# Kernel tuning notes

Measured on AMD Instinct MI355X. Metric: run time of the kernel, lower is better.

The kernel has to match this reference:

```python
import jax, jax.numpy as jnp
import numpy as np

B, S, D = 4, 2048, 1024
H = 16
HD = D // H

def setup_inputs() -> dict:
    key = jax.random.key(0)
    ks = jax.random.split(key, 6)
    std = 1.0 / np.sqrt(D)
    x = jax.random.normal(ks[0], (B, S, D), dtype=jnp.float32)
    Wq = jax.random.uniform(ks[1], (D, D), jnp.float32, -std, std)
    Wk = jax.random.uniform(ks[2], (D, D), jnp.float32, -std, std)
    Wv = jax.random.uniform(ks[3], (D, D), jnp.float32, -std, std)
    Wo = jax.random.uniform(ks[4], (D, D), jnp.float32, -std, std)
    bo = jax.random.uniform(ks[5], (D,), jnp.float32, -std, std)
    return {"x": x, "Wq": Wq, "Wk": Wk, "Wv": Wv, "Wo": Wo, "bo": bo}

def reference(x, Wq, Wk, Wv, Wo, bo):
    b, s, _ = x.shape
    # projections; torch Linear computes x @ W^T, here W stored as (d_in, d_out)... we use (D, D) applied as x @ W
    q = (x @ Wq).reshape(b, s, H, HD).transpose(0, 2, 1, 3)  # b h s hd
    k = (x @ Wk).reshape(b, s, H, HD).transpose(0, 2, 1, 3)
    v = (x @ Wv).reshape(b, s, H, HD).transpose(0, 2, 1, 3)
    scores = jnp.einsum('bhqd,bhkd->bhqk', q, k)
    causal = jnp.triu(jnp.ones((s, s), dtype=bool), k=1)
    scores = jnp.where(causal[None, None], -jnp.inf, scores)
    attn = jax.nn.softmax(scores / np.sqrt(HD), axis=-1)  # dropout=0.0 -> identity
    ctx = jnp.einsum('bhqk,bhkd->bhqd', attn, v)
    ctx = ctx.transpose(0, 2, 1, 3).reshape(b, s, D)
    return ctx @ Wo + bo
```

## Files before the change

kernel.cpp:

```cpp
#include <hip/hip_runtime.h>

typedef unsigned short u16;
typedef __bf16 bf16x8 __attribute__((ext_vector_type(8)));
typedef float f32x4 __attribute__((ext_vector_type(4)));

#define Bn 4
#define Sn 2048
#define Dn 1024
#define Hn 16
#define HDn 64

__device__ inline u16 f2bf(float f) {
  unsigned u = __builtin_bit_cast(unsigned, f);
  u += 0x7fffu + ((u >> 16) & 1u);
  return (u16)(u >> 16);
}

__device__ __forceinline__ void gl2lds16(const u16* g, u16* l) {
  __builtin_amdgcn_global_load_lds(
      (const __attribute__((address_space(1))) unsigned int*)g,
      (__attribute__((address_space(3))) unsigned int*)l, 16, 0, 0);
}

__device__ __forceinline__ float fexp2(float x) {
  return __builtin_amdgcn_exp2f(x);
}

__device__ __forceinline__ unsigned pk_bf_trunc(float lo, float hi) {
  return __builtin_amdgcn_perm(__builtin_bit_cast(unsigned, hi),
                               __builtin_bit_cast(unsigned, lo), 0x07060302u);
}

__global__ __launch_bounds__(256) void cvt4(const float* __restrict__ in,
                                            u16* __restrict__ out, int n4) {
  int i = blockIdx.x * 256 + threadIdx.x;
  if (i < n4) {
    float4 v = ((const float4*)in)[i];
    ushort4 o;
    o.x = f2bf(v.x); o.y = f2bf(v.y); o.z = f2bf(v.z); o.w = f2bf(v.w);
    ((ushort4*)out)[i] = o;
  }
}

__global__ __launch_bounds__(256) void tcvt4(const float* __restrict__ w0,
                                             const float* __restrict__ w1,
                                             const float* __restrict__ w2,
                                             const float* __restrict__ w3,
                                             u16* __restrict__ out) {
  __shared__ u16 tile[32][33];
  const float* in = (blockIdx.z == 0) ? w0 : (blockIdx.z == 1) ? w1
                   : (blockIdx.z == 2) ? w2 : w3;
  u16* dst = out + (size_t)blockIdx.z * Dn * Dn;
  int bx = blockIdx.x * 32;
  int by = blockIdx.y * 32;
  int tx = threadIdx.x & 31;
  int ty = threadIdx.x >> 5;
#pragma unroll
  for (int r = 0; r < 32; r += 8)
    tile[ty + r][tx] = f2bf(in[(size_t)(by + ty + r) * Dn + bx + tx]);
  __syncthreads();
#pragma unroll
  for (int r = 0; r < 32; r += 8)
    dst[(size_t)(bx + ty + r) * Dn + by + tx] = tile[tx][ty + r];
}

#define MFMA16(a, b, c) __builtin_amdgcn_mfma_f32_16x16x32_bf16(a, b, c, 0, 0, 0)

#define SRCP_INIT(APTR, BPTR)                                                \
  const u16* srcp[3][2];                                                     \
  _Pragma("unroll") for (int rg = 0; rg < 3; rg++) {                         \
    _Pragma("unroll") for (int j = 0; j < 2; j++) {                          \
      int o = j * 8192 + tid * 16;                                           \
      int l = o ^ (((o >> 8) & 7) << 4);                                     \
      int rho = l >> 7;                                                      \
      int c2 = (l >> 1) & 63;                                                \
      int gr;                                                                \
      if (rg == 0)      gr = bm + rho;                                       \
      else if (rg == 1) gr = bn + ((rho >> 5) << 6) + (rho & 31);            \
      else              gr = bn + ((rho >> 5) << 6) + 32 + (rho & 31);       \
      const u16* base = (rg == 0) ? (APTR) : (BPTR);                         \
      srcp[rg][j] = base + (size_t)gr * Dn + c2;                             \
    }                                                                        \
  }

#define ARD(D, Q, F, K)                                                      \
  (*(const bf16x8*)((const char*)&S[D][0][0] +                               \
      ((wr * 64 + (Q) * 32 + (F) * 16 + lcol) * 128 + ((K) ? cs1 : cs0))))
#define BRD(D, NI, K)                                                        \
  (*(const bf16x8*)((const char*)&S[D][1 + ((NI) >> 1)][0] +                 \
      ((wc * 32 + ((NI) & 1) * 16 + lcol) * 128 + ((K) ? cs1 : cs0))))

#define VM6 asm volatile("s_waitcnt vmcnt(6)" ::: "memory")
#define VM0 asm volatile("s_waitcnt vmcnt(0)" ::: "memory")

#define KTILE(D, DN, T, WAIT)                                                \
  {                                                                          \
    stg(0, DN, (T) + 2); stg(1, DN, (T) + 2); stg(2, DN, (T) + 2);           \
    __builtin_amdgcn_sched_barrier(0);                                       \
    bf16x8 a00 = ARD(D, 0, 0, 0), a10 = ARD(D, 0, 1, 0);                     \
    bf16x8 a20 = ARD(D, 1, 0, 0), a30 = ARD(D, 1, 1, 0);                     \
    bf16x8 bk0[4], bk1[4];                                                   \
    _Pragma("unroll") for (int ni = 0; ni < 4; ni++) bk0[ni] = BRD(D, ni, 0);\
    bf16x8 a01 = ARD(D, 0, 0, 1), a11 = ARD(D, 0, 1, 1);                     \
    bf16x8 a21 = ARD(D, 1, 0, 1), a31 = ARD(D, 1, 1, 1);                     \
    _Pragma("unroll") for (int ni = 0; ni < 4; ni++) bk1[ni] = BRD(D, ni, 1);\
    __builtin_amdgcn_s_setprio(1);                                           \
    _Pragma("unroll") for (int ni = 0; ni < 4; ni++) {                       \
      acc[0][ni] = MFMA16(a00, bk0[ni], acc[0][ni]);                         \
      acc[1][ni] = MFMA16(a10, bk0[ni], acc[1][ni]);                         \
      acc[2][ni] = MFMA16(a20, bk0[ni], acc[2][ni]);                         \
      acc[3][ni] = MFMA16(a30, bk0[ni], acc[3][ni]);                         \
    }                                                                        \
    _Pragma("unroll") for (int ni = 0; ni < 4; ni++) {                       \
      acc[0][ni] = MFMA16(a01, bk1[ni], acc[0][ni]);                         \
      acc[1][ni] = MFMA16(a11, bk1[ni], acc[1][ni]);                         \
      acc[2][ni] = MFMA16(a21, bk1[ni], acc[2][ni]);                         \
      acc[3][ni] = MFMA16(a31, bk1[ni], acc[3][ni]);                         \
    }                                                                        \
    __builtin_amdgcn_s_setprio(0);                                           \
    WAIT;                                                                    \
    __builtin_amdgcn_s_barrier();                                            \
    __builtin_amdgcn_sched_barrier(0);                                       \
  }

#define KLOOP                                                                \
  stg(0, 0, 0); stg(1, 0, 0); stg(2, 0, 0);                                  \
  stg(0, 1, 1); stg(1, 1, 1); stg(2, 1, 1);                                  \
  VM6;                                                                       \
  __builtin_amdgcn_s_barrier();                                              \
  __builtin_amdgcn_sched_barrier(0);                                         \
  _Pragma("unroll 1") for (int I = 0; I < 5; ++I) {                          \
    const int T0 = 3 * I;                                                    \
    KTILE(0, 2, T0, VM6)                                                     \
    KTILE(1, 0, T0 + 1, VM6)                                                 \
    KTILE(2, 1, T0 + 2, if (I == 4) { VM0; } else { VM6; })                  \
  }                                                                          \
  KTILE(0, 2, 15, )

__global__ __launch_bounds__(512, 2) void gemm_qkv(const u16* __restrict__ A,
                                                   const u16* __restrict__ Bt,
                                                   u16* __restrict__ qkb,
                                                   u16* __restrict__ vt,
                                                   float qscale) {
  __shared__ __attribute__((aligned(16))) u16 S[3][3][8192];

  const int tid = threadIdx.x;
  const int lane = tid & 63;
  const int lcol = lane & 15;
  const int quad = lane >> 4;
  const int wave = tid >> 6;
  const int wr = wave >> 2;
  const int wc = wave & 3;

  const int bid = blockIdx.x;
  const int idx = bid >> 3;
  const int bm = (((bid & 7) << 3) + (idx & 7)) * 128;
  const int bn = (idx >> 3) * 256;

  SRCP_INIT(A, Bt)

  auto stg = [&](int rg, int buf, int tile) {
    if (tile >= 16) return;
    const int k0 = tile << 6;
    u16* d = &S[buf][rg][tid * 8];
    gl2lds16(srcp[rg][0] + k0, d);
    gl2lds16(srcp[rg][1] + k0, d + 4096);
  };

  f32x4 acc[4][4];
#pragma unroll
  for (int i = 0; i < 4; i++)
#pragma unroll
    for (int j = 0; j < 4; j++) acc[i][j] = (f32x4){0.f, 0.f, 0.f, 0.f};

  const int SW = (lcol & 14) << 3;
  const int cs0 = (quad * 16) ^ SW;
  const int cs1 = (64 + quad * 16) ^ SW;

  KLOOP

  const int rb = bm + wr * 64 + quad * 4;
  const int cb = bn + wc * 64 + lcol;
  if (bn >= 2048) {
#pragma unroll
    for (int mi = 0; mi < 4; mi++) {
#pragma unroll
      for (int ni = 0; ni < 4; ni++) {
        int row0 = rb + mi * 16;
        int s = row0 & (Sn - 1);
        int bb = row0 >> 11;
        int vcol = cb + ni * 16 - 2048;
        int bh = (bb << 4) + (vcol >> 6);
        int hd = vcol & 63;
        unsigned d0 = (unsigned)f2bf(acc[mi][ni][0]) |
                      ((unsigned)f2bf(acc[mi][ni][1]) << 16);
        unsigned d1 = (unsigned)f2bf(acc[mi][ni][2]) |
                      ((unsigned)f2bf(acc[mi][ni][3]) << 16);
        *(uint2*)(vt + ((size_t)bh * HDn + hd) * Sn + s) = (uint2){d0, d1};
      }
    }
  } else {
    const float scale = (bn < 1024) ? qscale : 1.0f;
#pragma unroll
    for (int mi = 0; mi < 4; mi++) {
#pragma unroll
      for (int ni = 0; ni < 4; ni++) {
        int row0 = rb + mi * 16;
        int col = cb + ni * 16;
#pragma unroll
        for (int r = 0; r < 4; r++)
          qkb[(size_t)(row0 + r) * 2048 + col] = f2bf(acc[mi][ni][r] * scale);
      }
    }
  }
}

__global__ __launch_bounds__(512, 2) void gemm_out(const u16* __restrict__ A,
                                                   const u16* __restrict__ Bt,
                                                   float* __restrict__ Cout,
                                                   const float* __restrict__ bias) {
  __shared__ __attribute__((aligned(16))) u16 S[3][3][8192];

  const int tid = threadIdx.x;
  const int lane = tid & 63;
  const int lcol = lane & 15;
  const int quad = lane >> 4;
  const int wave = tid >> 6;
  const int wr = wave >> 2;
  const int wc = wave & 3;

  const int bid = blockIdx.x;
  const int idx = bid >> 3;
  const int bm = (((bid & 7) << 3) + (idx & 7)) * 128;
  const int bn = (idx >> 3) * 256;

  SRCP_INIT(A, Bt)

  auto stg = [&](int rg, int buf, int tile) {
    if (tile >= 16) return;
    const int k0 = tile << 6;
    u16* d = &S[buf][rg][tid * 8];
    gl2lds16(srcp[rg][0] + k0, d);
    gl2lds16(srcp[rg][1] + k0, d + 4096);
  };

  f32x4 acc[4][4];
#pragma unroll
  for (int i = 0; i < 4; i++)
#pragma unroll
    for (int j = 0; j < 4; j++) acc[i][j] = (f32x4){0.f, 0.f, 0.f, 0.f};

  const int SW = (lcol & 14) << 3;
  const int cs0 = (quad * 16) ^ SW;
  const int cs1 = (64 + quad * 16) ^ SW;

  KLOOP

  const int rb = bm + wr * 64 + quad * 4;
  const int cb = bn + wc * 64 + lcol;
  float bv[4];
#pragma unroll
  for (int ni = 0; ni < 4; ni++) bv[ni] = bias[cb + ni * 16];
#pragma unroll
  for (int mi = 0; mi < 4; mi++) {
#pragma unroll
    for (int ni = 0; ni < 4; ni++) {
      int row0 = rb + mi * 16;
      int col = cb + ni * 16;
#pragma unroll
      for (int r = 0; r < 4; r++)
        Cout[(size_t)(row0 + r) * Dn + col] = acc[mi][ni][r] + bv[ni];
    }
  }
}

__global__ __launch_bounds__(256, 2) void attn5(const u16* __restrict__ QK,
                                                const u16* __restrict__ Vt,
                                                u16* __restrict__ ctx) {
  __shared__ __attribute__((aligned(16))) u16 Ks2[2][2][64][32];
  __shared__ __attribute__((aligned(16))) u16 Vts2[2][2][64][32];
  __shared__ __attribute__((aligned(16))) u16 Pt[2][4][32][72];

  const int bh = blockIdx.x;
  const int b = bh >> 4, h = bh & 15;
  const int pair = blockIdx.y;
  const int t = threadIdx.x;
  const int w = t >> 6;
  const int lane = t & 63;
  const int lcol = lane & 15;
  const int quad = lane >> 4;
  const int qw0 = pair * 128 + w * 32;
  const int qw1 = (15 - pair) * 128 + w * 32;

  const size_t qkbase = ((size_t)b * Sn) * 2048 + h * HDn;
  const size_t obase = ((size_t)b * Sn) * Dn + h * HDn;
  const size_t vbase = ((size_t)bh * HDn) * Sn;

  bf16x8 qf[2][2][2];
#pragma unroll
  for (int si = 0; si < 2; si++) {
    const int qws = si ? qw1 : qw0;
#pragma unroll
    for (int qb = 0; qb < 2; qb++) {
      const u16* qp = QK + qkbase + (size_t)(qws + qb * 16 + lcol) * 2048 + quad * 8;
      qf[si][qb][0] = *(const bf16x8*)qp;
      qf[si][qb][1] = *(const bf16x8*)(qp + 32);
    }
  }

  bf16x8 onesf;
#pragma unroll
  for (int i = 0; i < 8; i++) onesf[i] = (__bf16)1.0f;

  f32x4 o[2][2][4];
  f32x4 ls[2][2];
#pragma unroll
  for (int si = 0; si < 2; si++) {
#pragma unroll
    for (int qb = 0; qb < 2; qb++) {
      ls[si][qb] = (f32x4){0.f, 0.f, 0.f, 0.f};
#pragma unroll
      for (int nb = 0; nb < 4; nb++) o[si][qb][nb] = (f32x4){0.f, 0.f, 0.f, 0.f};
    }
  }

  const int srow = lane >> 2;
  const int sseg = ((lane & 3) ^ ((lane >> 3) & 3)) * 8;
  const u16* kp0 = QK + qkbase + 1024 + (size_t)(w * 16 + srow) * 2048 + sseg;
  const u16* vp0 = Vt + vbase + (size_t)(w * 16 + srow) * Sn + sseg;
  u16* ksl = &Ks2[0][0][0][0] + w * 512 + lane * 8;
  u16* vsl = &Vts2[0][0][0][0] + w * 512 + lane * 8;

  const int rsw = (quad ^ ((lcol >> 1) & 3)) * 8;

  auto stg_kv = [&](int bs, int j0) {
    const u16* kp = kp0 + (size_t)j0 * 2048;
    const u16* vp = vp0 + j0;
    u16* kd = ksl + bs * 4096;
    u16* vd = vsl + bs * 4096;
    gl2lds16(kp, kd);
    gl2lds16(kp + 32, kd + 2048);
    gl2lds16(vp, vd);
    gl2lds16(vp + 32, vd + 2048);
  };

  auto qk_strip = [&](int si, f32x4 (*s)[2], int bs) {
    __builtin_amdgcn_s_setprio(1);
#pragma unroll
    for (int mb = 0; mb < 4; mb++) {
      bf16x8 kf0 = *(const bf16x8*)(&Ks2[bs][0][mb * 16 + lcol][rsw]);
      bf16x8 kf1 = *(const bf16x8*)(&Ks2[bs][1][mb * 16 + lcol][rsw]);
#pragma unroll
      for (int qb = 0; qb < 2; qb++) {
        f32x4 a = (f32x4){0.f, 0.f, 0.f, 0.f};
        a = MFMA16(kf0, qf[si][qb][0], a);
        a = MFMA16(kf1, qf[si][qb][1], a);
        s[mb][qb] = a;
      }
    }
    __builtin_amdgcn_s_setprio(0);
  };

  auto sm_strip = [&](int si, int qw, int j0, f32x4 (*s)[2]) {
    const bool needmask = (j0 + 63 > qw);
#pragma unroll
    for (int qb = 0; qb < 2; qb++) {
      const int qrow = qw + qb * 16 + lcol;
#pragma unroll
      for (int mb = 0; mb < 4; mb++) {
        float p[4];
#pragma unroll
        for (int r = 0; r < 4; r++) p[r] = fexp2(s[mb][qb][r]);
        if (needmask) {
          const int kvb = j0 + mb * 16 + quad * 4;
#pragma unroll
          for (int r = 0; r < 4; r++)
            if (kvb + r > qrow) p[r] = 0.f;
        }
        unsigned d0 = pk_bf_trunc(p[0], p[1]);
        unsigned d1 = pk_bf_trunc(p[2], p[3]);
        *(uint2*)(&Pt[si][w][qb * 16 + lcol][mb * 16 + quad * 4]) = (uint2){d0, d1};
      }
    }
  };

  auto pv_strip = [&](int si, int bs) {
    __builtin_amdgcn_s_setprio(1);
#pragma unroll
    for (int c = 0; c < 2; c++) {
      bf16x8 pf0 = *(const bf16x8*)(&Pt[si][w][lcol][c * 32 + quad * 8]);
      bf16x8 pf1 = *(const bf16x8*)(&Pt[si][w][16 + lcol][c * 32 + quad * 8]);
      ls[si][0] = MFMA16(onesf, pf0, ls[si][0]);
      ls[si][1] = MFMA16(onesf, pf1, ls[si][1]);
#pragma unroll
      for (int nb = 0; nb < 4; nb++) {
        bf16x8 vf = *(const bf16x8*)(&Vts2[bs][c][nb * 16 + lcol][rsw]);
        o[si][0][nb] = MFMA16(vf, pf0, o[si][0][nb]);
        o[si][1][nb] = MFMA16(vf, pf1, o[si][1][nb]);
      }
    }
    __builtin_amdgcn_s_setprio(0);
  };

  const int n_kv = (15 - pair) * 128 + 128;
  const int nit = n_kv >> 6;

  stg_kv(0, 0);
#pragma unroll 1
  for (int it = 0; it < nit; ++it) {
    const int j0 = it << 6;
    const int bs = it & 1;
    if (it + 1 < nit) {
      stg_kv(bs ^ 1, j0 + 64);
      asm volatile("s_waitcnt vmcnt(4)" ::: "memory");
    } else {
      asm volatile("s_waitcnt vmcnt(0)" ::: "memory");
    }
    __builtin_amdgcn_s_barrier();
    __builtin_amdgcn_sched_barrier(0);

    const bool a0 = (j0 <= qw0 + 31);
    f32x4 s1[4][2], s0[4][2];
    qk_strip(1, s1, bs);
    if (a0) qk_strip(0, s0, bs);
    sm_strip(1, qw1, j0, s1);
    if (a0) sm_strip(0, qw0, j0, s0);
    pv_strip(1, bs);
    if (a0) pv_strip(0, bs);

    __builtin_amdgcn_s_barrier();
    __builtin_amdgcn_sched_barrier(0);
  }

#pragma unroll
  for (int si = 0; si < 2; si++) {
    const int qws = si ? qw1 : qw0;
#pragma unroll
    for (int qb = 0; qb < 2; qb++) {
      float inv = 1.0f / ls[si][qb][0];
#pragma unroll
      for (int nb = 0; nb < 4; nb++) {
        unsigned d0 = (unsigned)f2bf(o[si][qb][nb][0] * inv) |
                      ((unsigned)f2bf(o[si][qb][nb][1] * inv) << 16);
        unsigned d1 = (unsigned)f2bf(o[si][qb][nb][2] * inv) |
                      ((unsigned)f2bf(o[si][qb][nb][3] * inv) << 16);
        u16* p = ctx + obase + (size_t)(qws + qb * 16 + lcol) * Dn + nb * 16 + quad * 4;
        *(uint2*)p = (uint2){d0, d1};
      }
    }
  }
}

extern "C" void kernel_launch(void* const* d_in, const int* in_sizes, int n_in,
                              void* d_out, int out_size, void* d_ws, size_t ws_size,
                              hipStream_t stream) {
  const float* x  = (const float*)d_in[0];
  const float* Wq = (const float*)d_in[1];
  const float* Wk = (const float*)d_in[2];
  const float* Wv = (const float*)d_in[3];
  const float* Wo = (const float*)d_in[4];
  const float* bo = (const float*)d_in[5];
  float* out = (float*)d_out;

  const size_t BSD = (size_t)Bn * Sn * Dn;
  const size_t DD = (size_t)Dn * Dn;

  u16* xb    = (u16*)d_ws;
  u16* wall  = xb + BSD;
  u16* qkb   = wall + 4 * DD;
  u16* vt    = qkb + 2 * BSD;
  u16* cb    = vt + BSD;

  cvt4<<<(int)(BSD / 4 / 256), 256, 0, stream>>>(x, xb, (int)(BSD / 4));
  tcvt4<<<dim3(Dn / 32, Dn / 32, 4), 256, 0, stream>>>(Wq, Wk, Wv, Wo, wall);

  gemm_qkv<<<dim3(768), 512, 0, stream>>>(xb, wall, qkb, vt,
                                          0.125f * 1.44269504f);

  attn5<<<dim3(Bn * Hn, 8), 256, 0, stream>>>(qkb, vt, cb);

  gemm_out<<<dim3(256), 512, 0, stream>>>(cb, wall + 3 * DD, out, bo);
}
```

Baseline: 233.9 us.

## Enlarge QKV GEMM tile to 256x256 with double-buffered LDS pipeline

The QKV projection GEMM moves from 128x256 tiles with triple buffering to 256x256 tiles with double buffering, so each wave computes a 128x64 output block (8x4 MFMA accumulators) and the grid halves to 384 blocks. The larger tile raises arithmetic intensity and reuses each LDS fragment more often, cutting global and LDS traffic per FLOP. The cost is a full vmcnt(0) wait each k-step, which means less load/compute overlap, plus higher register pressure from 128 accumulator floats per thread. With 384 blocks on 256 CUs, the last wave of work is also unevenly balanced.

Measured after the change: 292.2 us. 1.25x slower.

```diff
diff --git a/kernel.cpp b/kernel.cpp
--- a/kernel.cpp
+++ b/kernel.cpp
@@ -65,6 +65,147 @@
 }
 
 #define MFMA16(a, b, c) __builtin_amdgcn_mfma_f32_16x16x32_bf16(a, b, c, 0, 0, 0)
+#define VM6 asm volatile("s_waitcnt vmcnt(6)" ::: "memory")
+#define VM0 asm volatile("s_waitcnt vmcnt(0)" ::: "memory")
+
+__global__ __launch_bounds__(512, 2) void gemm_qkv(const u16* __restrict__ A,
+                                                   const u16* __restrict__ Bt,
+                                                   u16* __restrict__ qkb,
+                                                   u16* __restrict__ vt,
+                                                   float qscale) {
+  __shared__ __attribute__((aligned(16))) u16 S[2][4][8192];
+
+  const int tid = threadIdx.x;
+  const int lane = tid & 63;
+  const int lcol = lane & 15;
+  const int quad = lane >> 4;
+  const int wave = tid >> 6;
+  const int wr = wave >> 2;
+  const int wc = wave & 3;
+
+  const int bid = blockIdx.x;
+  const int idx = bid >> 3;
+  const int bm = (((bid & 7) << 2) + (idx & 3)) * 256;
+  const int bn = (idx >> 2) * 256;
+
+  const u16* srcp[4][2];
+#pragma unroll
+  for (int rg = 0; rg < 4; rg++) {
+#pragma unroll
+    for (int j = 0; j < 2; j++) {
+      int o = j * 8192 + tid * 16;
+      int l = o ^ (((o >> 8) & 7) << 4);
+      int rho = l >> 7;
+      int c2 = (l >> 1) & 63;
+      int gr;
+      if (rg == 0)      gr = bm + rho;
+      else if (rg == 1) gr = bm + 128 + rho;
+      else if (rg == 2) gr = bn + rho;
+      else              gr = bn + 128 + rho;
+      const u16* base = (rg < 2) ? A : Bt;
+      srcp[rg][j] = base + (size_t)gr * Dn + c2;
+    }
+  }
+
+  auto stg = [&](int rg, int buf, int tile) {
+    if (tile >= 16) return;
+    const int k0 = tile << 6;
+    u16* d = &S[buf][rg][tid * 8];
+    gl2lds16(srcp[rg][0] + k0, d);
+    gl2lds16(srcp[rg][1] + k0, d + 4096);
+  };
+
+  f32x4 acc[8][4];
+#pragma unroll
+  for (int i = 0; i < 8; i++)
+#pragma unroll
+    for (int j = 0; j < 4; j++) acc[i][j] = (f32x4){0.f, 0.f, 0.f, 0.f};
+
+  const int SW = (lcol & 14) << 3;
+  const int cs0 = (quad * 16) ^ SW;
+  const int cs1 = (64 + quad * 16) ^ SW;
+
+#define AR2(D, MI, K)                                                        \
+  (*(const bf16x8*)((const char*)&S[D][wr][0] +                              \
+      (((MI) * 16 + lcol) * 128 + ((K) ? cs1 : cs0))))
+#define BR2(D, NI, K)                                                        \
+  (*(const bf16x8*)((const char*)&S[D][2 + (wc >> 1)][0] +                   \
+      ((((wc & 1) * 64 + (NI) * 16 + lcol)) * 128 + ((K) ? cs1 : cs0))))
+
+#define KSTEP2(D, K)                                                         \
+  {                                                                          \
+    bf16x8 af[8], bf[4];                                                     \
+    _Pragma("unroll") for (int mi = 0; mi < 8; mi++) af[mi] = AR2(D, mi, K); \
+    _Pragma("unroll") for (int ni = 0; ni < 4; ni++) bf[ni] = BR2(D, ni, K); \
+    __builtin_amdgcn_s_setprio(1);                                           \
+    _Pragma("unroll") for (int ni = 0; ni < 4; ni++)                         \
+      _Pragma("unroll") for (int mi = 0; mi < 8; mi++)                       \
+        acc[mi][ni] = MFMA16(af[mi], bf[ni], acc[mi][ni]);                   \
+    __builtin_amdgcn_s_setprio(0);                                           \
+  }
+
+#define KT2(D, T)                                                            \
+  {                                                                          \
+    stg(0, (D) ^ 1, (T) + 1); stg(1, (D) ^ 1, (T) + 1);                      \
+    stg(2, (D) ^ 1, (T) + 1); stg(3, (D) ^ 1, (T) + 1);                      \
+    __builtin_amdgcn_sched_barrier(0);                                       \
+    KSTEP2(D, 0)                                                             \
+    KSTEP2(D, 1)                                                             \
+    VM0;                                                                     \
+    __builtin_amdgcn_s_barrier();                                            \
+    __builtin_amdgcn_sched_barrier(0);                                       \
+  }
+
+  stg(0, 0, 0); stg(1, 0, 0); stg(2, 0, 0); stg(3, 0, 0);
+  VM0;
+  __builtin_amdgcn_s_barrier();
+  __builtin_amdgcn_sched_barrier(0);
+
+#pragma unroll 1
+  for (int I = 0; I < 8; ++I) {
+    KT2(0, 2 * I)
+    KT2(1, 2 * I + 1)
+  }
+#undef KT2
+#undef KSTEP2
+#undef AR2
+#undef BR2
+
+  const int rb = bm + wr * 128 + quad * 4;
+  const int cb = bn + wc * 64 + lcol;
+  if (bn >= 2048) {
+#pragma unroll
+    for (int ai = 0; ai < 8; ai++) {
+#pragma unroll
+      for (int bj = 0; bj < 4; bj++) {
+        int row0 = rb + ai * 16;
+        int s = row0 & (Sn - 1);
+        int bb = row0 >> 11;
+        int vcol = cb + bj * 16 - 2048;
+        int bh = (bb << 4) + (vcol >> 6);
+        int hd = vcol & 63;
+        unsigned d0 = (unsigned)f2bf(acc[ai][bj][0]) |
+                      ((unsigned)f2bf(acc[ai][bj][1]) << 16);
+        unsigned d1 = (unsigned)f2bf(acc[ai][bj][2]) |
+                      ((unsigned)f2bf(acc[ai][bj][3]) << 16);
+        *(uint2*)(vt + ((size_t)bh * HDn + hd) * Sn + s) = (uint2){d0, d1};
+      }
+    }
+  } else {
+    const float scale = (bn < 1024) ? qscale : 1.0f;
+#pragma unroll
+    for (int ai = 0; ai < 8; ai++) {
+#pragma unroll
+      for (int bj = 0; bj < 4; bj++) {
+        int row0 = rb + ai * 16;
+        int col = cb + bj * 16;
+#pragma unroll
+        for (int r = 0; r < 4; r++)
+          qkb[(size_t)(row0 + r) * 2048 + col] = f2bf(acc[ai][bj][r] * scale);
+      }
+    }
+  }
+}
 
 #define SRCP_INIT(APTR, BPTR)                                                \
   const u16* srcp[3][2];                                                     \
@@ -89,9 +230,6 @@
 #define BRD(D, NI, K)                                                        \
   (*(const bf16x8*)((const char*)&S[D][1 + ((NI) >> 1)][0] +                 \
       ((wc * 32 + ((NI) & 1) * 16 + lcol) * 128 + ((K) ? cs1 : cs0))))
-
-#define VM6 asm volatile("s_waitcnt vmcnt(6)" ::: "memory")
-#define VM0 asm volatile("s_waitcnt vmcnt(0)" ::: "memory")
 
 #define KTILE(D, DN, T, WAIT)                                                \
   {                                                                          \
@@ -137,84 +275,6 @@
   }                                                                          \
   KTILE(0, 2, 15, )
 
-__global__ __launch_bounds__(512, 2) void gemm_qkv(const u16* __restrict__ A,
-                                                   const u16* __restrict__ Bt,
-                                                   u16* __restrict__ qkb,
-                                                   u16* __restrict__ vt,
-                                                   float qscale) {
-  __shared__ __attribute__((aligned(16))) u16 S[3][3][8192];
-
-  const int tid = threadIdx.x;
-  const int lane = tid & 63;
-  const int lcol = lane & 15;
-  const int quad = lane >> 4;
-  const int wave = tid >> 6;
-  const int wr = wave >> 2;
-  const int wc = wave & 3;
-
-  const int bid = blockIdx.x;
-  const int idx = bid >> 3;
-  const int bm = (((bid & 7) << 3) + (idx & 7)) * 128;
-  const int bn = (idx >> 3) * 256;
-
-  SRCP_INIT(A, Bt)
-
-  auto stg = [&](int rg, int buf, int tile) {
-    if (tile >= 16) return;
-    const int k0 = tile << 6;
-    u16* d = &S[buf][rg][tid * 8];
-    gl2lds16(srcp[rg][0] + k0, d);
-    gl2lds16(srcp[rg][1] + k0, d + 4096);
-  };
-
-  f32x4 acc[4][4];
-#pragma unroll
-  for (int i = 0; i < 4; i++)
-#pragma unroll
-    for (int j = 0; j < 4; j++) acc[i][j] = (f32x4){0.f, 0.f, 0.f, 0.f};
-
-  const int SW = (lcol & 14) << 3;
-  const int cs0 = (quad * 16) ^ SW;
-  const int cs1 = (64 + quad * 16) ^ SW;
-
-  KLOOP
-
-  const int rb = bm + wr * 64 + quad * 4;
-  const int cb = bn + wc * 64 + lcol;
-  if (bn >= 2048) {
-#pragma unroll
-    for (int mi = 0; mi < 4; mi++) {
-#pragma unroll
-      for (int ni = 0; ni < 4; ni++) {
-        int row0 = rb + mi * 16;
-        int s = row0 & (Sn - 1);
-        int bb = row0 >> 11;
-        int vcol = cb + ni * 16 - 2048;
-        int bh = (bb << 4) + (vcol >> 6);
-        int hd = vcol & 63;
-        unsigned d0 = (unsigned)f2bf(acc[mi][ni][0]) |
-                      ((unsigned)f2bf(acc[mi][ni][1]) << 16);
-        unsigned d1 = (unsigned)f2bf(acc[mi][ni][2]) |
-                      ((unsigned)f2bf(acc[mi][ni][3]) << 16);
-        *(uint2*)(vt + ((size_t)bh * HDn + hd) * Sn + s) = (uint2){d0, d1};
-      }
-    }
-  } else {
-    const float scale = (bn < 1024) ? qscale : 1.0f;
-#pragma unroll
-    for (int mi = 0; mi < 4; mi++) {
-#pragma unroll
-      for (int ni = 0; ni < 4; ni++) {
-        int row0 = rb + mi * 16;
-        int col = cb + ni * 16;
-#pragma unroll
-        for (int r = 0; r < 4; r++)
-          qkb[(size_t)(row0 + r) * 2048 + col] = f2bf(acc[mi][ni][r] * scale);
-      }
-    }
-  }
-}
-
 __global__ __launch_bounds__(512, 2) void gemm_out(const u16* __restrict__ A,
                                                    const u16* __restrict__ Bt,
                                                    float* __restrict__ Cout,
@@ -474,7 +534,7 @@
   cvt4<<<(int)(BSD / 4 / 256), 256, 0, stream>>>(x, xb, (int)(BSD / 4));
   tcvt4<<<dim3(Dn / 32, Dn / 32, 4), 256, 0, stream>>>(Wq, Wk, Wv, Wo, wall);
 
-  gemm_qkv<<<dim3(768), 512, 0, stream>>>(xb, wall, qkb, vt,
+  gemm_qkv<<<dim3(384), 512, 0, stream>>>(xb, wall, qkb, vt,
                                           0.125f * 1.44269504f);
 
   attn5<<<dim3(Bn * Hn, 8), 256, 0, stream>>>(qkb, vt, cb);
```
